# Kernel optimization log

Hardware: AMD Instinct MI355X
Metric: run time of the kernel (lower is better)

Reference implementation:

```python
import jax, jax.numpy as jnp
import numpy as np


def _quat2euler_xyz(q):
    # q: [B,4] -> euler angles (x, y, z), order 'xyz' as in the torch code
    q0, q1, q2, q3 = q[..., 0], q[..., 1], q[..., 2], q[..., 3]
    x = jnp.arctan2(2 * (q0 * q1 + q2 * q3), 1 - 2 * (q1 * q1 + q2 * q2))
    y = jnp.arcsin(jnp.clip(2 * (q0 * q2 - q1 * q3), -1.0, 1.0))
    z = jnp.arctan2(2 * (q0 * q3 + q1 * q2), 1 - 2 * (q2 * q2 + q3 * q3))
    return x, y, z


def _quat2rmat(q):
    # Batched version of the per-sample loop: R = (R1 @ R2 @ R3)^T, [B,3,3]
    ax, ay, az = _quat2euler_xyz(q)
    cx, sx = jnp.cos(ax), jnp.sin(ax)
    cy, sy = jnp.cos(ay), jnp.sin(ay)
    cz, sz = jnp.cos(az), jnp.sin(az)
    o = jnp.ones_like(cx)
    z0 = jnp.zeros_like(cx)
    r1 = jnp.stack([jnp.stack([o, z0, z0], -1),
                    jnp.stack([z0, cx, sx], -1),
                    jnp.stack([z0, -sx, cx], -1)], -2)
    r2 = jnp.stack([jnp.stack([cy, z0, -sy], -1),
                    jnp.stack([z0, o, z0], -1),
                    jnp.stack([sy, z0, cy], -1)], -2)
    r3 = jnp.stack([jnp.stack([cz, sz, z0], -1),
                    jnp.stack([-sz, cz, z0], -1),
                    jnp.stack([z0, z0, o], -1)], -2)
    return jnp.swapaxes(r1 @ r2 @ r3, -1, -2)


def _extrin_mat(t, q):
    # t: [B,3], q: [B,4] -> [R | R t] of shape [B,3,4]
    R = _quat2rmat(q)
    rt = jnp.einsum('bij,bj->bi', R, t)
    return jnp.concatenate([R, rt[..., None]], axis=-1)


def _project_im2ground(cam_mat, X, mask):
    # cam_mat: [B,3,4]; keep columns [0,1,3] and pseudo-invert (3x3)
    cam3 = jnp.take(cam_mat, jnp.array([0, 1, 3]), axis=2)      # [B,3,3]
    pinv = jnp.linalg.pinv(cam3)                                  # [B,3,3]
    homo = jnp.concatenate([X, jnp.ones_like(X[..., :1])], -1)    # [B,T,3]
    p = jnp.einsum('bij,btj->bti', pinv, homo)                    # [B,T,3]
    denom = jnp.where(mask[..., None], p[..., 2:3], 1.0)          # safe divide for masked pts
    return p[..., :2] / denom                                     # [B,T,2]


def reference(X, y, y_pred, intrin_mat):
    # y_pred <- cat(y[:, :2], y_pred) to make a full Nx7 pose
    yp = jnp.concatenate([y[:, :2], y_pred], axis=1)              # [B,7]
    t_pred, q_pred = yp[:, :3], yp[:, 3:]
    q_pred_n = q_pred / jnp.linalg.norm(q_pred, axis=1, keepdims=True)
    t_lab, q_lab = y[:, :3], y[:, 3:]

    ex_pred = _extrin_mat(t_pred, q_pred_n)                       # [B,3,4]
    ex_lab = _extrin_mat(t_lab, q_lab)                            # [B,3,4]
    cam_pred = jnp.einsum('ij,bjk->bik', intrin_mat, ex_pred)     # [B,3,4]
    cam_lab = jnp.einsum('ij,bjk->bik', intrin_mat, ex_lab)

    # Validity mask: both pixel coords > 0. The torch code compacts valid points to
    # the front and zero-pads; since pred/label share the same mask, the sum of
    # per-point L2 norms is identical to masking in place.
    mask = (X[..., 0] > 0) & (X[..., 1] > 0)                      # [B,T]

    p3d_pred = _project_im2ground(cam_pred, X, mask)
    p3d_lab = _project_im2ground(cam_lab, X, mask)

    diff = jnp.where(mask[..., None], p3d_pred - p3d_lab, 0.0)    # [B,T,2]
    sumsq = jnp.sum(diff * diff, axis=-1)                         # [B,T]
    norms = jnp.where(mask, jnp.sqrt(jnp.where(mask, sumsq, 1.0)), 0.0)
    loss = jnp.mean(jnp.sum(norms, axis=-1))

    loss_t = jnp.mean(jnp.abs(yp[:, :3] - y[:, :3]))              # .item() in torch -> detached
    loss_r = jnp.mean(jnp.abs(yp[:, 3:] - y[:, 3:]))
    return jnp.stack([loss, jax.lax.stop_gradient(loss_t), jax.lax.stop_gradient(loss_r)])


def setup_inputs() -> dict:
    key = jax.random.key(0)
    kx, kt, kq, kp = jax.random.split(key, 4)
    B, T = 8192, 1024
    # Pixel-like coordinates; some negative so the validity mask is non-trivial
    X = jax.random.normal(kx, (B, T, 2), dtype=jnp.float32) * 400.0 + 300.0
    t = jax.random.normal(kt, (B, 3), dtype=jnp.float32)
    q = jax.random.normal(kq, (B, 4), dtype=jnp.float32)
    q = q / jnp.linalg.norm(q, axis=1, keepdims=True)             # unit label quaternion
    y = jnp.concatenate([t, q], axis=1)                           # [B,7]
    y_pred = jax.random.normal(kp, (B, 5), dtype=jnp.float32)     # [z_t, quat(4)]
    FX = FY = 1000.0
    CX, CY = 640.0, 360.0
    intrin_mat = jnp.array([[FX, 0.0, CX], [0.0, FY, CY], [0.0, 0.0, 1.0]], dtype=jnp.float32)
    return {"X": X, "y": y, "y_pred": y_pred, "intrin_mat": intrin_mat}
```

## Files before the change

### kernel.cpp

```cpp
#include <hip/hip_runtime.h>


namespace {
constexpr int kB = 8192;
constexpr int kT = 1024;
constexpr double kEpsF32 = 1.1920928955078125e-07;
constexpr size_t kPinvDoubles = (size_t)kB * 18;
}

__global__ __launch_bounds__(64) void geo_setup(
    const float* __restrict__ y, const float* __restrict__ yp,
    const float* __restrict__ K, double* __restrict__ pinvs) {
  int m = blockIdx.x * 64 + threadIdx.x;
  if (m >= kB * 2) return;
  int b = m >> 1;
  bool pred = (m & 1) == 0;
  const float* yb = y + b * 7;
  float t0, t1, t2, q0, q1, q2, q3;
  if (pred) {
    const float* pb = yp + b * 5;
    t0 = yb[0]; t1 = yb[1]; t2 = pb[0];
    q0 = pb[1]; q1 = pb[2]; q2 = pb[3]; q3 = pb[4];
    float n = sqrtf(q0*q0 + q1*q1 + q2*q2 + q3*q3);
    q0 /= n; q1 /= n; q2 /= n; q3 /= n;
  } else {
    t0 = yb[0]; t1 = yb[1]; t2 = yb[2];
    q0 = yb[3]; q1 = yb[4]; q2 = yb[5]; q3 = yb[6];
  }

  float s1f = 2.f*(q0*q1 + q2*q3);
  float c1f = 1.f - 2.f*(q1*q1 + q2*q2);
  float h1 = sqrtf(fmaxf(s1f*s1f + c1f*c1f, 1e-30f));
  float cxa = c1f/h1, sxa = s1f/h1;
  float syf = fminf(1.f, fmaxf(-1.f, 2.f*(q0*q2 - q1*q3)));
  float cyf = sqrtf(fmaxf(0.f, 1.f - syf*syf));
  float s3f = 2.f*(q0*q3 + q1*q2);
  float c3f = 1.f - 2.f*(q2*q2 + q3*q3);
  float h3 = sqrtf(fmaxf(s3f*s3f + c3f*c3f, 1e-30f));
  float cza = c3f/h3, sza = s3f/h3;

  float R00 = cyf*cza, R01 = sxa*syf*cza - cxa*sza, R02 = cxa*syf*cza + sxa*sza;
  float R10 = cyf*sza, R11 = sxa*syf*sza + cxa*cza, R12 = cxa*syf*sza - sxa*cza;
  float R20 = -syf,    R21 = sxa*cyf,               R22 = cxa*cyf;

  float rt0 = R00*t0 + R01*t1 + R02*t2;
  float rt1 = R10*t0 + R11*t1 + R12*t2;
  float rt2 = R20*t0 + R21*t1 + R22*t2;

  float K0=K[0],K1=K[1],K2=K[2],K3=K[3],K4=K[4],K5=K[5],K6=K[6],K7=K[7],K8=K[8];
  float a00f = K0*R00 + K1*R10 + K2*R20, a01f = K0*R01 + K1*R11 + K2*R21, a02f = K0*rt0 + K1*rt1 + K2*rt2;
  float a10f = K3*R00 + K4*R10 + K5*R20, a11f = K3*R01 + K4*R11 + K5*R21, a12f = K3*rt0 + K4*rt1 + K5*rt2;
  float a20f = K6*R00 + K7*R10 + K8*R20, a21f = K6*R01 + K7*R11 + K8*R21, a22f = K6*rt0 + K7*rt1 + K8*rt2;

  double a00=a00f,a01=a01f,a02=a02f,a10=a10f,a11=a11f,a12=a12f,a20=a20f,a21=a21f,a22=a22f;

  double m00 = a00*a00 + a10*a10 + a20*a20;
  double m01 = a00*a01 + a10*a11 + a20*a21;
  double m02 = a00*a02 + a10*a12 + a20*a22;
  double m11 = a01*a01 + a11*a11 + a21*a21;
  double m12 = a01*a02 + a11*a12 + a21*a22;
  double m22 = a02*a02 + a12*a12 + a22*a22;

  double qm = (m00 + m11 + m22) / 3.0;
  double d00 = m00 - qm, d11 = m11 - qm, d22 = m22 - qm;
  double p2 = d00*d00 + d11*d11 + d22*d22 + 2.0*(m01*m01 + m02*m02 + m12*m12);
  double pp = sqrt(fmax(p2 / 6.0, 1e-300));
  double ib = 1.0 / pp;
  double n00 = d00*ib, n01 = m01*ib, n02 = m02*ib;
  double n11 = d11*ib, n12 = m12*ib, n22 = d22*ib;
  double detN = n00*(n11*n22 - n12*n12) - n01*(n01*n22 - n12*n02) + n02*(n01*n12 - n11*n02);
  double r = fmin(1.0, fmax(-1.0, 0.5 * detN));
  double phi = acos(r) / 3.0;
  double lam1 = qm + 2.0*pp*cos(phi);
  double lam3t = qm + 2.0*pp*cos(phi + 2.0943951023931953);
  double lam2 = 3.0*qm - lam1 - lam3t;

  double s1v = sqrt(fmax(lam1, 1e-300));
  double s2v = sqrt(fmax(lam2, 1e-300));
  double detA = a00*(a11*a22 - a12*a21) - a01*(a10*a22 - a12*a20) + a02*(a10*a21 - a11*a20);
  double s3est = fabs(detA) / (s1v * s2v);

  double floorS = 2.0 * kEpsF32 * s1v;

  double P[9];
  if (s3est >= floorS) {
    double c00 = a11*a22 - a12*a21, c01 = a02*a21 - a01*a22, c02 = a01*a12 - a02*a11;
    double c10 = a12*a20 - a10*a22, c11 = a00*a22 - a02*a20, c12 = a02*a10 - a00*a12;
    double c20 = a10*a21 - a11*a20, c21 = a01*a20 - a00*a21, c22 = a00*a11 - a01*a10;
    double rd = 1.0 / detA;
    P[0]=c00*rd; P[1]=c01*rd; P[2]=c02*rd;
    P[3]=c10*rd; P[4]=c11*rd; P[5]=c12*rd;
    P[6]=c20*rd; P[7]=c21*rd; P[8]=c22*rd;
  } else {
    double lam3a = (detA * detA) / (lam1 * lam2);
    double N00 = m00 - lam3a, N11 = m11 - lam3a, N22 = m22 - lam3a;
    double cx0 = m01*m12 - m02*N11, cy0 = m02*m01 - N00*m12, cz0 = N00*N11 - m01*m01;
    double cx1 = N11*N22 - m12*m12, cy1 = m12*m02 - m01*N22, cz1 = m01*m12 - N11*m02;
    double cx2 = m12*m02 - N22*m01, cy2 = N22*N00 - m02*m02, cz2 = m02*m01 - m12*N00;
    double q0n = cx0*cx0 + cy0*cy0 + cz0*cz0;
    double q1n = cx1*cx1 + cy1*cy1 + cz1*cz1;
    double q2n = cx2*cx2 + cy2*cy2 + cz2*cz2;
    double vx = cx0, vy = cy0, vz = cz0, qn = q0n;
    if (q1n > qn) { vx = cx1; vy = cy1; vz = cz1; qn = q1n; }
    if (q2n > qn) { vx = cx2; vy = cy2; vz = cz2; qn = q2n; }
    double invn = 1.0 / sqrt(fmax(qn, 1e-300));
    vx *= invn; vy *= invn; vz *= invn;

    double w0a = a00*vx + a01*vy + a02*vz;
    double w1a = a10*vx + a11*vy + a12*vz;
    double w2a = a20*vx + a21*vy + a22*vz;
    double s3v = sqrt(fmax(w0a*w0a + w1a*w1a + w2a*w2a, 1e-300));
    double s3hat = fmax(s3v, floorS);

    double B00 = m00 + lam1*vx*vx, B01 = m01 + lam1*vx*vy, B02 = m02 + lam1*vx*vz;
    double B11 = m11 + lam1*vy*vy, B12 = m12 + lam1*vy*vz, B22 = m22 + lam1*vz*vz;
    double i00 = B11*B22 - B12*B12;
    double i01 = B02*B12 - B01*B22;
    double i02 = B01*B12 - B02*B11;
    double i11 = B00*B22 - B02*B02;
    double i12 = B01*B02 - B00*B12;
    double i22 = B00*B11 - B01*B01;
    double dB = B00*i00 + B01*i01 + B02*i02;
    double rB = 1.0 / dB;
    double Bi00=i00*rB, Bi01=i01*rB, Bi02=i02*rB, Bi11=i11*rB, Bi12=i12*rB, Bi22=i22*rB;
    double u0 = Bi00*vx + Bi01*vy + Bi02*vz;
    double u1 = Bi01*vx + Bi11*vy + Bi12*vz;
    double u2 = Bi02*vx + Bi12*vy + Bi22*vz;
    double Mp00 = Bi00 - u0*vx, Mp01 = Bi01 - u0*vy, Mp02 = Bi02 - u0*vz;
    double Mp10 = Bi01 - u1*vx, Mp11 = Bi11 - u1*vy, Mp12 = Bi12 - u1*vz;
    double Mp20 = Bi02 - u2*vx, Mp21 = Bi12 - u2*vy, Mp22 = Bi22 - u2*vz;
    P[0] = Mp00*a00 + Mp01*a01 + Mp02*a02;
    P[1] = Mp00*a10 + Mp01*a11 + Mp02*a12;
    P[2] = Mp00*a20 + Mp01*a21 + Mp02*a22;
    P[3] = Mp10*a00 + Mp11*a01 + Mp12*a02;
    P[4] = Mp10*a10 + Mp11*a11 + Mp12*a12;
    P[5] = Mp10*a20 + Mp11*a21 + Mp12*a22;
    P[6] = Mp20*a00 + Mp21*a01 + Mp22*a02;
    P[7] = Mp20*a10 + Mp21*a11 + Mp22*a12;
    P[8] = Mp20*a20 + Mp21*a21 + Mp22*a22;
    double f = 1.0 / (s3hat * s3v);
    P[0] += vx*w0a*f; P[1] += vx*w1a*f; P[2] += vx*w2a*f;
    P[3] += vy*w0a*f; P[4] += vy*w1a*f; P[5] += vy*w2a*f;
    P[6] += vz*w0a*f; P[7] += vz*w1a*f; P[8] += vz*w2a*f;
  }

  double* out = pinvs + ((size_t)b * 18 + (pred ? 0 : 9));
#pragma unroll
  for (int i = 0; i < 9; ++i) out[i] = P[i];
}

__global__ __launch_bounds__(256) void geo_main(
    const float* __restrict__ X, const double* __restrict__ pinvs,
    double* __restrict__ partial) {
  const int b = blockIdx.x;
  const int tid = threadIdx.x;
  __shared__ double Md[18];
  __shared__ float  Mf[18];
  __shared__ double wsum[4];

  if (tid < 18) {
    double v = pinvs[(size_t)b * 18 + tid];
    Md[tid] = v;
    Mf[tid] = (float)v;
  }
  __syncthreads();

  float P0=Mf[0],P1=Mf[1],P2=Mf[2],P3=Mf[3],P4=Mf[4],P5=Mf[5],P6=Mf[6],P7=Mf[7],P8=Mf[8];
  float L0=Mf[9],L1=Mf[10],L2=Mf[11],L3=Mf[12],L4=Mf[13],L5=Mf[14],L6=Mf[15],L7=Mf[16],L8=Mf[17];

  auto pt = [&](float px, float py) -> double {
    bool mask = (px > 0.f) && (py > 0.f);
    if (!mask) return 0.0;
    float cp = fmaf(P6, px, fmaf(P7, py, P8));
    float cl = fmaf(L6, px, fmaf(L7, py, L8));
    float magp = fabsf(P6*px) + fabsf(P7*py) + fabsf(P8);
    float magl = fabsf(L6*px) + fabsf(L7*py) + fabsf(L8);
    if (fabsf(cp) < 0.03f*magp || fabsf(cl) < 0.03f*magl) {
      double x = (double)px, yv = (double)py;
      double apd = Md[0]*x + Md[1]*yv + Md[2];
      double bpd = Md[3]*x + Md[4]*yv + Md[5];
      double cpd = Md[6]*x + Md[7]*yv + Md[8];
      double ald = Md[9]*x  + Md[10]*yv + Md[11];
      double bld = Md[12]*x + Md[13]*yv + Md[14];
      double cld = Md[15]*x + Md[16]*yv + Md[17];
      double du = apd/cpd - ald/cld;
      double dv = bpd/cpd - bld/cld;
      return sqrt(du*du + dv*dv);
    }
    float ap = fmaf(P0, px, fmaf(P1, py, P2));
    float bp = fmaf(P3, px, fmaf(P4, py, P5));
    float al = fmaf(L0, px, fmaf(L1, py, L2));
    float bl = fmaf(L3, px, fmaf(L4, py, L5));
    float du = ap/cp - al/cl;
    float dv = bp/cp - bl/cl;
    return (double)sqrtf(du*du + dv*dv);
  };

  const float4* Xr = (const float4*)(X + (size_t)b * (2 * kT));
  double local = 0.0;
#pragma unroll
  for (int it = 0; it < 2; ++it) {
    float4 v = Xr[tid + it * 256];
    local += pt(v.x, v.y);
    local += pt(v.z, v.w);
  }

#pragma unroll
  for (int off = 32; off > 0; off >>= 1)
    local += __shfl_down(local, off);
  if ((tid & 63) == 0) wsum[tid >> 6] = local;
  __syncthreads();
  if (tid == 0)
    partial[b] = wsum[0] + wsum[1] + wsum[2] + wsum[3];
}

__global__ __launch_bounds__(1024) void geo_reduce(
    const double* __restrict__ partial, const float* __restrict__ y,
    const float* __restrict__ yp, float* __restrict__ out) {
  const int tid = threadIdx.x;
  __shared__ double red[16][3];

  double s = 0.0, lt = 0.0, lr = 0.0;
  for (int b = tid; b < kB; b += 1024) {
    s += partial[b];
    const float* yb = y + b * 7;
    const float* pb = yp + b * 5;
    lt += fabs((double)pb[0] - (double)yb[2]);
    lr += fabs((double)pb[1] - (double)yb[3]) + fabs((double)pb[2] - (double)yb[4]) +
          fabs((double)pb[3] - (double)yb[5]) + fabs((double)pb[4] - (double)yb[6]);
  }
#pragma unroll
  for (int off = 32; off > 0; off >>= 1) {
    s  += __shfl_down(s, off);
    lt += __shfl_down(lt, off);
    lr += __shfl_down(lr, off);
  }
  if ((tid & 63) == 0) {
    int w = tid >> 6;
    red[w][0] = s; red[w][1] = lt; red[w][2] = lr;
  }
  __syncthreads();
  if (tid == 0) {
    double ts = 0, tl = 0, tr = 0;
#pragma unroll
    for (int w = 0; w < 16; ++w) { ts += red[w][0]; tl += red[w][1]; tr += red[w][2]; }
    out[0] = (float)(ts / (double)kB);
    out[1] = (float)(tl / (3.0 * (double)kB));
    out[2] = (float)(tr / (4.0 * (double)kB));
  }
}

extern "C" void kernel_launch(void* const* d_in, const int* in_sizes, int n_in,
                              void* d_out, int out_size, void* d_ws, size_t ws_size,
                              hipStream_t stream) {
  const float* X  = (const float*)d_in[0];
  const float* y  = (const float*)d_in[1];
  const float* yp = (const float*)d_in[2];
  const float* K  = (const float*)d_in[3];

  double* pinvs = (double*)d_ws;
  double* partial = pinvs + kPinvDoubles;

  geo_setup<<<(kB * 2 + 63) / 64, 64, 0, stream>>>(y, yp, K, pinvs);
  geo_main<<<kB, 256, 0, stream>>>(X, pinvs, partial);
  geo_reduce<<<1, 1024, 0, stream>>>(partial, y, yp, (float*)d_out);
}
```

Measured before the change: 134.4 us.

## Fuse final reduction into main kernel via last-block atomic counter; cheaper reciprocals

Removes the separate single-block reduce kernel by having each main block bump an atomic counter, with the last block doing the final sum and the loss_t/loss_r terms. The counter is reset in the setup kernel. In the per-point math it precomputes absolute matrix entries so the magnitude check uses FMAs, and it replaces two float divisions with a hardware reciprocal plus one Newton step. This saves a kernel launch and some ALU work, at the cost of a threadfence and atomic per block, a serial tail in the last block, and slightly different rounding in the fast path.

```diff
diff --git a/kernel.cpp b/kernel.cpp
--- a/kernel.cpp
+++ b/kernel.cpp
@@ -10,8 +10,10 @@
 
 __global__ __launch_bounds__(64) void geo_setup(
     const float* __restrict__ y, const float* __restrict__ yp,
-    const float* __restrict__ K, double* __restrict__ pinvs) {
+    const float* __restrict__ K, double* __restrict__ pinvs,
+    unsigned int* __restrict__ count) {
   int m = blockIdx.x * 64 + threadIdx.x;
+  if (m == 0) *count = 0;
   if (m >= kB * 2) return;
   int b = m >> 1;
   bool pred = (m & 1) == 0;
@@ -151,12 +153,15 @@
 
 __global__ __launch_bounds__(256) void geo_main(
     const float* __restrict__ X, const double* __restrict__ pinvs,
-    double* __restrict__ partial) {
+    double* __restrict__ partial, unsigned int* __restrict__ count,
+    const float* __restrict__ y, const float* __restrict__ yp,
+    float* __restrict__ out) {
   const int b = blockIdx.x;
   const int tid = threadIdx.x;
   __shared__ double Md[18];
   __shared__ float  Mf[18];
   __shared__ double wsum[4];
+  __shared__ bool isLast;
 
   if (tid < 18) {
     double v = pinvs[(size_t)b * 18 + tid];
@@ -165,16 +170,17 @@
   }
   __syncthreads();
 
-  float P0=Mf[0],P1=Mf[1],P2=Mf[2],P3=Mf[3],P4=Mf[4],P5=Mf[5],P6=Mf[6],P7=Mf[7],P8=Mf[8];
-  float L0=Mf[9],L1=Mf[10],L2=Mf[11],L3=Mf[12],L4=Mf[13],L5=Mf[14],L6=Mf[15],L7=Mf[16],L8=Mf[17];
+  const float P0=Mf[0],P1=Mf[1],P2=Mf[2],P3=Mf[3],P4=Mf[4],P5=Mf[5],P6=Mf[6],P7=Mf[7],P8=Mf[8];
+  const float L0=Mf[9],L1=Mf[10],L2=Mf[11],L3=Mf[12],L4=Mf[13],L5=Mf[14],L6=Mf[15],L7=Mf[16],L8=Mf[17];
+  const float AP6=fabsf(P6),AP7=fabsf(P7),AP8=fabsf(P8);
+  const float AL6=fabsf(L6),AL7=fabsf(L7),AL8=fabsf(L8);
 
   auto pt = [&](float px, float py) -> double {
-    bool mask = (px > 0.f) && (py > 0.f);
-    if (!mask) return 0.0;
+    if (!((px > 0.f) && (py > 0.f))) return 0.0;
     float cp = fmaf(P6, px, fmaf(P7, py, P8));
     float cl = fmaf(L6, px, fmaf(L7, py, L8));
-    float magp = fabsf(P6*px) + fabsf(P7*py) + fabsf(P8);
-    float magl = fabsf(L6*px) + fabsf(L7*py) + fabsf(L8);
+    float magp = fmaf(AP6, px, fmaf(AP7, py, AP8));
+    float magl = fmaf(AL6, px, fmaf(AL7, py, AL8));
     if (fabsf(cp) < 0.03f*magp || fabsf(cl) < 0.03f*magl) {
       double x = (double)px, yv = (double)py;
       double apd = Md[0]*x + Md[1]*yv + Md[2];
@@ -191,9 +197,11 @@
     float bp = fmaf(P3, px, fmaf(P4, py, P5));
     float al = fmaf(L0, px, fmaf(L1, py, L2));
     float bl = fmaf(L3, px, fmaf(L4, py, L5));
-    float du = ap/cp - al/cl;
-    float dv = bp/cp - bl/cl;
-    return (double)sqrtf(du*du + dv*dv);
+    float rp = __builtin_amdgcn_rcpf(cp); rp = rp * fmaf(-cp, rp, 2.0f);
+    float rl = __builtin_amdgcn_rcpf(cl); rl = rl * fmaf(-cl, rl, 2.0f);
+    float du = fmaf(ap, rp, -(al*rl));
+    float dv = fmaf(bp, rp, -(bl*rl));
+    return (double)sqrtf(fmaf(du, du, dv*dv));
   };
 
   const float4* Xr = (const float4*)(X + (size_t)b * (2 * kT));
@@ -210,43 +218,45 @@
     local += __shfl_down(local, off);
   if ((tid & 63) == 0) wsum[tid >> 6] = local;
   __syncthreads();
-  if (tid == 0)
+  if (tid == 0) {
     partial[b] = wsum[0] + wsum[1] + wsum[2] + wsum[3];
-}
-
-__global__ __launch_bounds__(1024) void geo_reduce(
-    const double* __restrict__ partial, const float* __restrict__ y,
-    const float* __restrict__ yp, float* __restrict__ out) {
-  const int tid = threadIdx.x;
-  __shared__ double red[16][3];
-
-  double s = 0.0, lt = 0.0, lr = 0.0;
-  for (int b = tid; b < kB; b += 1024) {
-    s += partial[b];
-    const float* yb = y + b * 7;
-    const float* pb = yp + b * 5;
-    lt += fabs((double)pb[0] - (double)yb[2]);
-    lr += fabs((double)pb[1] - (double)yb[3]) + fabs((double)pb[2] - (double)yb[4]) +
-          fabs((double)pb[3] - (double)yb[5]) + fabs((double)pb[4] - (double)yb[6]);
-  }
-#pragma unroll
-  for (int off = 32; off > 0; off >>= 1) {
-    s  += __shfl_down(s, off);
-    lt += __shfl_down(lt, off);
-    lr += __shfl_down(lr, off);
-  }
-  if ((tid & 63) == 0) {
-    int w = tid >> 6;
-    red[w][0] = s; red[w][1] = lt; red[w][2] = lr;
+    __threadfence();
+    unsigned int prev = atomicAdd(count, 1u);
+    isLast = (prev == (unsigned int)(gridDim.x - 1));
   }
   __syncthreads();
-  if (tid == 0) {
-    double ts = 0, tl = 0, tr = 0;
-#pragma unroll
-    for (int w = 0; w < 16; ++w) { ts += red[w][0]; tl += red[w][1]; tr += red[w][2]; }
-    out[0] = (float)(ts / (double)kB);
-    out[1] = (float)(tl / (3.0 * (double)kB));
-    out[2] = (float)(tr / (4.0 * (double)kB));
+
+  if (isLast) {
+    __threadfence();
+    double s = 0.0, lt = 0.0, lr = 0.0;
+    for (int i = tid; i < kB; i += 256) {
+      s += partial[i];
+      const float* yb = y + i * 7;
+      const float* pb = yp + i * 5;
+      lt += fabs((double)pb[0] - (double)yb[2]);
+      lr += fabs((double)pb[1] - (double)yb[3]) + fabs((double)pb[2] - (double)yb[4]) +
+            fabs((double)pb[3] - (double)yb[5]) + fabs((double)pb[4] - (double)yb[6]);
+    }
+    __shared__ double red[4][3];
+#pragma unroll
+    for (int off = 32; off > 0; off >>= 1) {
+      s  += __shfl_down(s, off);
+      lt += __shfl_down(lt, off);
+      lr += __shfl_down(lr, off);
+    }
+    if ((tid & 63) == 0) {
+      int w = tid >> 6;
+      red[w][0] = s; red[w][1] = lt; red[w][2] = lr;
+    }
+    __syncthreads();
+    if (tid == 0) {
+      double ts = 0, tl = 0, tr = 0;
+#pragma unroll
+      for (int w = 0; w < 4; ++w) { ts += red[w][0]; tl += red[w][1]; tr += red[w][2]; }
+      out[0] = (float)(ts / (double)kB);
+      out[1] = (float)(tl / (3.0 * (double)kB));
+      out[2] = (float)(tr / (4.0 * (double)kB));
+    }
   }
 }
 
@@ -260,8 +270,8 @@
 
   double* pinvs = (double*)d_ws;
   double* partial = pinvs + kPinvDoubles;
-
-  geo_setup<<<(kB * 2 + 63) / 64, 64, 0, stream>>>(y, yp, K, pinvs);
-  geo_main<<<kB, 256, 0, stream>>>(X, pinvs, partial);
-  geo_reduce<<<1, 1024, 0, stream>>>(partial, y, yp, (float*)d_out);
-}
+  unsigned int* count = (unsigned int*)(partial + kB);
+
+  geo_setup<<<(kB * 2 + 63) / 64, 64, 0, stream>>>(y, yp, K, pinvs, count);
+  geo_main<<<kB, 256, 0, stream>>>(X, pinvs, partial, count, y, yp, (float*)d_out);
+}
```

New measurement: 317.4 us. 136% more time.
